# Kernel tuning notes

Measured on AMD Instinct MI355X. Metric: run time of the kernel, lower is better.

## Reference

```python
import jax, jax.numpy as jnp
import numpy as np
import math

B, L, D, H, FF = 4, 1024, 1024, 16, 4096
DH = D // H
EPS = 1e-12


def layer_norm(x, gamma, beta):
    mean = x.mean(-1, keepdims=True)
    var = ((x - mean) ** 2).mean(-1, keepdims=True)  # biased var, matches unbiased=False
    return gamma * (x - mean) / jnp.sqrt(var + EPS) + beta


def setup_inputs() -> dict:
    key = jax.random.key(0)
    ks = jax.random.split(key, 16)
    s = 0.02
    return {
        "x": jax.random.normal(ks[0], (B, L, D), jnp.float32),
        "attn_bias": jax.random.uniform(ks[1], (B, L, L), jnp.float32),
        "src_mask": jax.random.randint(ks[2], (B, L), 0, 2, jnp.int32),
        "wq": jax.random.normal(ks[3], (D, D), jnp.float32) * s,
        "bq": jnp.zeros((D,), jnp.float32),
        "wk": jax.random.normal(ks[4], (D, D), jnp.float32) * s,
        "bk": jnp.zeros((D,), jnp.float32),
        "wv": jax.random.normal(ks[5], (D, D), jnp.float32) * s,
        "bv": jnp.zeros((D,), jnp.float32),
        "wo": jax.random.normal(ks[6], (D, D), jnp.float32) * s,
        "bo": jnp.zeros((D,), jnp.float32),
        "gamma1": jnp.ones((D,), jnp.float32),
        "beta1": jnp.zeros((D,), jnp.float32),
        "w1": jax.random.normal(ks[7], (D, FF), jnp.float32) * s,
        "b1": jnp.zeros((FF,), jnp.float32),
        "w2": jax.random.normal(ks[8], (FF, D), jnp.float32) * s,
        "b2": jnp.zeros((D,), jnp.float32),
        "gamma2": jnp.ones((D,), jnp.float32),
        "beta2": jnp.zeros((D,), jnp.float32),
    }


def reference(x, attn_bias, src_mask, wq, bq, wk, bk, wv, bv, wo, bo,
              gamma1, beta1, w1, b1, w2, b2, gamma2, beta2):
    # ---- multi-head attention with multiplicative bias + additive mask ----
    def split_heads(t):  # [B,L,D] -> [B,H,L,DH]
        return t.reshape(B, L, H, DH).transpose(0, 2, 1, 3)

    q = split_heads(x @ wq + bq)
    k = split_heads(x @ wk + bk)
    v = split_heads(x @ wv + bv)

    score = jnp.einsum('bhqd,bhkd->bhqk', q, k) / math.sqrt(DH)
    score = score * attn_bias[:, None, :, :]               # multiplicative bias
    score = jnp.where(src_mask[:, None, None, :] == 0, -10000.0, score)
    p = jax.nn.softmax(score, axis=-1)
    ctx = jnp.einsum('bhqk,bhkd->bhqd', p, v)
    ctx = ctx.transpose(0, 2, 1, 3).reshape(B, L, D)
    attn_out = ctx @ wo + bo

    h = layer_norm(x + attn_out, gamma1, beta1)

    # ---- position-wise FFN ----
    ffn = jax.nn.relu(h @ w1 + b1) @ w2 + b2
    out = layer_norm(h + ffn, gamma2, beta2)
    return out
```

## Files before the change

### kernel.cpp

```cpp
#include <hip/hip_runtime.h>
#include <hip/hip_bf16.h>
#include <math.h>

#define BB 4
#define LL 1024
#define DD 1024
#define HH 16
#define DHH 64
#define FFF 4096
#define MM (BB*LL)
#define LDQ 3072

typedef __attribute__((ext_vector_type(8))) short short8;
typedef __attribute__((ext_vector_type(4))) float f32x4;

__device__ __forceinline__ ushort f2bf(float f) {
    __hip_bfloat16 h = __float2bfloat16(f);
    return *(ushort*)&h;
}
__device__ __forceinline__ float bf2f(ushort u) {
    __hip_bfloat16 h = *(__hip_bfloat16*)&u;
    return __bfloat162float(h);
}
__device__ __forceinline__ float fexp2(float x) {
#if __has_builtin(__builtin_amdgcn_exp2f)
    return __builtin_amdgcn_exp2f(x);
#else
    return exp2f(x);
#endif
}

__device__ __forceinline__ float block_reduce_sum(float v, float* red, int tid) {
    red[tid] = v;
    __syncthreads();
    for (int off = 128; off > 0; off >>= 1) {
        if (tid < off) red[tid] += red[tid + off];
        __syncthreads();
    }
    float r = red[0];
    __syncthreads();
    return r;
}

__global__ __launch_bounds__(256)
void cast_bf16(const float* __restrict__ in, ushort* __restrict__ out) {
    const int i = blockIdx.x * 256 + threadIdx.x;
    float4 v = ((const float4*)in)[i];
    ushort4 o;
    o.x = f2bf(v.x); o.y = f2bf(v.y); o.z = f2bf(v.z); o.w = f2bf(v.w);
    ((ushort4*)out)[i] = o;
}

__global__ __launch_bounds__(256)
void swizzle_bias(const float* __restrict__ bias, float* __restrict__ B) {
    __shared__ float rowbuf[1024];
    const int row = blockIdx.x;
    const int t = threadIdx.x;
    *(float4*)&rowbuf[t * 4] = *(const float4*)&bias[(size_t)row * 1024 + t * 4];
    __syncthreads();
    const int kt = t >> 4, c = t & 15;
    const float s = 1.4426950408889634f;
    float4 o;
    o.x = rowbuf[kt * 64 + 0 * 16 + c] * s;
    o.y = rowbuf[kt * 64 + 1 * 16 + c] * s;
    o.z = rowbuf[kt * 64 + 2 * 16 + c] * s;
    o.w = rowbuf[kt * 64 + 3 * 16 + c] * s;
    *(float4*)&B[(size_t)row * 1024 + t * 4] = o;
}

__global__ __launch_bounds__(256)
void transpose_cast(const float* __restrict__ W, ushort* __restrict__ WT,
                    int K, int N) {
    __shared__ float tile[32][33];
    const int n0 = blockIdx.x * 32, k0 = blockIdx.y * 32;
    const int t = threadIdx.x;
    const int r = t >> 3, c4 = (t & 7) * 4;
    float4 v = *(const float4*)&W[(size_t)(k0 + r) * N + n0 + c4];
    tile[r][c4 + 0] = v.x; tile[r][c4 + 1] = v.y;
    tile[r][c4 + 2] = v.z; tile[r][c4 + 3] = v.w;
    __syncthreads();
    ushort4 o;
    o.x = f2bf(tile[c4 + 0][r]);
    o.y = f2bf(tile[c4 + 1][r]);
    o.z = f2bf(tile[c4 + 2][r]);
    o.w = f2bf(tile[c4 + 3][r]);
    *(ushort4*)&WT[(size_t)(n0 + r) * K + k0 + c4] = o;
}

__global__ __launch_bounds__(256)
void concat3(const float* __restrict__ a, const float* __restrict__ b,
             const float* __restrict__ c, float* __restrict__ o) {
    const int i = blockIdx.x * 256 + threadIdx.x;
    o[i] = (i < 1024) ? a[i] : ((i < 2048) ? b[i - 1024] : c[i - 2048]);
}

template<int BN>
__global__ __launch_bounds__(256)
void gemm_bf16_sk(const ushort* __restrict__ A, const ushort* __restrict__ Bt,
                  float* __restrict__ P, int M, int N, int K) {
    constexpr int JF = BN / 32;
    __shared__ ushort Als0[128 * 32];
    __shared__ ushort Als1[128 * 32];
    __shared__ ushort Bls0[BN * 32];
    __shared__ ushort Bls1[BN * 32];

    const int L = blockIdx.x + gridDim.x * blockIdx.y;
    const int xcd = L & 7;
    const int idx = L >> 3;
    const int mpx = gridDim.y >> 3;
    const int bm = (xcd * mpx + (idx % mpx)) * 128;
    const int bn = (idx / mpx) * BN;
    const int kbeg = blockIdx.z * (K >> 1);
    const int kend = kbeg + (K >> 1);

    const int t = threadIdx.x;
    const int lane = t & 63;
    const int w = t >> 6;
    const int wm = (w >> 1) * 64;
    const int wn = (w & 1) * (BN / 2);
    const int fm = lane & 15;
    const int kg = lane >> 4;

    f32x4 acc[4][JF] = {};

    for (int k0 = kbeg; k0 < kend; k0 += 64) {
        #pragma unroll
        for (int j = 0; j < 2; ++j) {
            const int chunk = j * 256 + t;
            const int row = chunk >> 2, kc = chunk & 3;
            const ushort* ga0 = A + (size_t)(bm + row) * K + k0 + kc * 8;
            __builtin_amdgcn_global_load_lds(
                (const __attribute__((address_space(1))) void*)ga0,
                (__attribute__((address_space(3))) void*)(Als0 + chunk * 8), 16, 0, 0);
            const ushort* ga1 = ga0 + 32;
            __builtin_amdgcn_global_load_lds(
                (const __attribute__((address_space(1))) void*)ga1,
                (__attribute__((address_space(3))) void*)(Als1 + chunk * 8), 16, 0, 0);
        }
        #pragma unroll
        for (int j = 0; j < BN / 64; ++j) {
            const int chunk = j * 256 + t;
            const int row = chunk >> 2, kc = chunk & 3;
            const ushort* gb0 = Bt + (size_t)(bn + row) * K + k0 + kc * 8;
            __builtin_amdgcn_global_load_lds(
                (const __attribute__((address_space(1))) void*)gb0,
                (__attribute__((address_space(3))) void*)(Bls0 + chunk * 8), 16, 0, 0);
            const ushort* gb1 = gb0 + 32;
            __builtin_amdgcn_global_load_lds(
                (const __attribute__((address_space(1))) void*)gb1,
                (__attribute__((address_space(3))) void*)(Bls1 + chunk * 8), 16, 0, 0);
        }
        __syncthreads();

        short8 af[4][2], bfr[JF][2];
        #pragma unroll
        for (int i = 0; i < 4; ++i) {
            af[i][0] = *(const short8*)&Als0[(wm + i * 16 + fm) * 32 + kg * 8];
            af[i][1] = *(const short8*)&Als1[(wm + i * 16 + fm) * 32 + kg * 8];
        }
        #pragma unroll
        for (int j = 0; j < JF; ++j) {
            bfr[j][0] = *(const short8*)&Bls0[(wn + j * 16 + fm) * 32 + kg * 8];
            bfr[j][1] = *(const short8*)&Bls1[(wn + j * 16 + fm) * 32 + kg * 8];
        }
        #pragma unroll
        for (int i = 0; i < 4; ++i)
            #pragma unroll
            for (int j = 0; j < JF; ++j) {
                acc[i][j] = __builtin_amdgcn_mfma_f32_16x16x32_bf16(
                    af[i][0], bfr[j][0], acc[i][j], 0, 0, 0);
                acc[i][j] = __builtin_amdgcn_mfma_f32_16x16x32_bf16(
                    af[i][1], bfr[j][1], acc[i][j], 0, 0, 0);
            }
        __syncthreads();
    }

    float* Pz = P + (size_t)blockIdx.z * M * N;
    const int orow0 = (lane >> 4) * 4;
    const int ocol = lane & 15;
    #pragma unroll
    for (int j = 0; j < JF; ++j) {
        const int n = bn + wn + j * 16 + ocol;
        #pragma unroll
        for (int i = 0; i < 4; ++i) {
            const int m0 = bm + wm + i * 16 + orow0;
            #pragma unroll
            for (int r = 0; r < 4; ++r)
                Pz[(size_t)(m0 + r) * N + n] = acc[i][j][r];
        }
    }
}


#define BARM() asm volatile("s_barrier" ::: "memory")
#define VMC4() asm volatile("s_waitcnt vmcnt(4)" ::: "memory")
#define LGK0() do { asm volatile("s_waitcnt lgkmcnt(0)" ::: "memory"); \
                    __builtin_amdgcn_sched_barrier(0); } while (0)

__device__ __forceinline__ short8 fragrd(const ushort* h, int row, int s, int kg) {
    const int cb = ((s << 6) + (kg << 4)) ^ ((row & 7) << 4);
    return *(const short8*)(h + row * 64 + (cb >> 1));
}

__device__ __forceinline__ void stage_half(const ushort* __restrict__ src,
                                           int srcK, ushort* ldsh, int t) {
    #pragma unroll
    for (int l = 0; l < 2; ++l) {
        const int chunk = l * 512 + t;
        const int r = chunk >> 3;
        const int cb_log = ((chunk & 7) * 16) ^ ((r & 7) << 4);
        const ushort* g = src + (size_t)r * srcK + (cb_log >> 1);
        __builtin_amdgcn_global_load_lds(
            (const __attribute__((address_space(1))) void*)g,
            (__attribute__((address_space(3))) void*)(ldsh + chunk * 8), 16, 0, 0);
    }
}

__global__ __launch_bounds__(512, 2)
void gemm256(const ushort* __restrict__ A, const ushort* __restrict__ Bt,
             const float* __restrict__ bias, ushort* __restrict__ C,
             ushort* __restrict__ Vt, int vn0,
             int M, int N, int K, int relu, int qlim) {
    __shared__ ushort lds[65536];

    const int nt = K >> 6;
    const int t = threadIdx.x;
    const int lane = t & 63;
    const int w = t >> 6;
    const int wr = w >> 2, wc = w & 3;
    const int fm = lane & 15, kg = lane >> 4;

    const int bid = blockIdx.x;
    const int wg = (bid & 7) * (gridDim.x >> 3) + (bid >> 3);
    const int bm = (wg & 15) << 8;
    const int bn = (wg >> 4) << 8;

    ushort* const A0 = lds;
    ushort* const B0 = lds + 16384;
    ushort* const A1 = lds + 32768;
    ushort* const B1 = lds + 49152;

    const ushort* const Ah0 = A0 + wr * 8192;
    const ushort* const Ah1 = A1 + wr * 8192;
    const ushort* const Bh0 = B0 + (wc >> 1) * 8192;
    const ushort* const Bh1 = B1 + (wc >> 1) * 8192;
    const int brow = (wc & 1) * 64;

    #define ASRC(tt, h) (A  + (size_t)(bm + (h) * 128) * K + (tt) * 64)
    #define BSRC(tt, h) (Bt + (size_t)(bn + (h) * 128) * K + (tt) * 64)

    f32x4 acc[8][4] = {};
    short8 af[4][2];
    short8 bf2[4][2];

    #define RD_A(HP, MI0) do { \
        _Pragma("unroll") \
        for (int i = 0; i < 4; ++i) { \
            const int row = ((MI0) + i) * 16 + fm; \
            af[i][0] = fragrd((HP), row, 0, kg); \
            af[i][1] = fragrd((HP), row, 1, kg); \
        } } while (0)

    #define RD_B(HP, J0) do { \
        _Pragma("unroll") \
        for (int jj = 0; jj < 2; ++jj) { \
            const int row = brow + ((J0) + jj) * 16 + fm; \
            bf2[(J0) + jj][0] = fragrd((HP), row, 0, kg); \
            bf2[(J0) + jj][1] = fragrd((HP), row, 1, kg); \
        } } while (0)

    #define QMFMA(MI0, J0) do { \
        __builtin_amdgcn_s_setprio(1); \
        _Pragma("unroll") \
        for (int i = 0; i < 4; ++i) { \
            _Pragma("unroll") \
            for (int jj = 0; jj < 2; ++jj) { \
                acc[(MI0)+i][(J0)+jj] = __builtin_amdgcn_mfma_f32_16x16x32_bf16( \
                    af[i][0], bf2[(J0)+jj][0], acc[(MI0)+i][(J0)+jj], 0, 0, 0); \
                acc[(MI0)+i][(J0)+jj] = __builtin_amdgcn_mfma_f32_16x16x32_bf16( \
                    af[i][1], bf2[(J0)+jj][1], acc[(MI0)+i][(J0)+jj], 0, 0, 0); \
            } } \
        __builtin_amdgcn_s_setprio(0); \
    } while (0)

    stage_half(BSRC(0, 0), K, B0, t);
    stage_half(BSRC(0, 1), K, B0 + 8192, t);
    stage_half(ASRC(0, 0), K, A0, t);
    stage_half(ASRC(0, 1), K, A0 + 8192, t);
    stage_half(BSRC(1, 0), K, B1, t);
    stage_half(BSRC(1, 1), K, B1 + 8192, t);
    VMC4();
    BARM();

    for (int it = 0; it < (nt >> 1); ++it) {
        const int ta = 2 * it;
        const int tb = ta + 1;
        const int t2 = min(ta + 2, nt - 1);
        const int t3 = min(ta + 3, nt - 1);

        RD_A(Ah0, 0); RD_B(Bh0, 0);
        stage_half(ASRC(tb, 0), K, A1, t);
        BARM(); LGK0(); QMFMA(0, 0); BARM();
        RD_B(Bh0, 2);
        stage_half(ASRC(tb, 1), K, A1 + 8192, t);
        BARM(); LGK0(); QMFMA(0, 2); BARM();
        RD_A(Ah0, 4);
        stage_half(BSRC(t2, 0), K, B0, t);
        BARM(); LGK0(); QMFMA(4, 2); BARM();
        stage_half(BSRC(t2, 1), K, B0 + 8192, t);
        VMC4();
        BARM(); LGK0(); QMFMA(4, 0); BARM();
        RD_A(Ah1, 0); RD_B(Bh1, 0);
        stage_half(ASRC(t2, 0), K, A0, t);
        BARM(); LGK0(); QMFMA(0, 0); BARM();
        RD_B(Bh1, 2);
        stage_half(ASRC(t2, 1), K, A0 + 8192, t);
        BARM(); LGK0(); QMFMA(0, 2); BARM();
        RD_A(Ah1, 4);
        stage_half(BSRC(t3, 0), K, B1, t);
        BARM(); LGK0(); QMFMA(4, 2); BARM();
        stage_half(BSRC(t3, 1), K, B1 + 8192, t);
        VMC4();
        BARM(); LGK0(); QMFMA(4, 0); BARM();
    }

    const int oc = lane & 15, og = lane >> 4;
    #pragma unroll
    for (int nj = 0; nj < 4; ++nj) {
        const int nb = bn + wc * 64 + nj * 16;
        const int n = nb + oc;
        const float bv = bias[n];
        const bool isV = nb >= vn0;
        #pragma unroll
        for (int mi = 0; mi < 8; ++mi) {
            const int m0 = bm + wr * 128 + mi * 16 + og * 4;
            if (isV) {
                ushort4 o;
                o.x = f2bf(acc[mi][nj][0] + bv);
                o.y = f2bf(acc[mi][nj][1] + bv);
                o.z = f2bf(acc[mi][nj][2] + bv);
                o.w = f2bf(acc[mi][nj][3] + bv);
                *(ushort4*)&Vt[((size_t)((m0 >> 10) << 10) + (n - vn0)) * 1024 + (m0 & 1023)] = o;
            } else {
                #pragma unroll
                for (int r = 0; r < 4; ++r) {
                    float v = acc[mi][nj][r] + bv;
                    if (relu) v = fmaxf(v, 0.0f);
                    if (n < qlim) v *= 0.125f;
                    C[(size_t)(m0 + r) * N + n] = f2bf(v);
                }
            }
        }
    }
    #undef ASRC
    #undef BSRC
    #undef RD_A
    #undef RD_B
    #undef QMFMA
}

__global__ __launch_bounds__(256, 4)
void attn_mfma(const ushort* __restrict__ QKVb, const ushort* __restrict__ Vt,
               const float* __restrict__ biasw, const int* __restrict__ mask,
               ushort* __restrict__ ctx) {
    const int q0 = blockIdx.x * 64;
    const int h = blockIdx.y;
    const int b = blockIdx.z;
    const int t = threadIdx.x;
    const int lane = t & 63;
    const int w = t >> 6;
    const int g = lane >> 4;
    const int c = lane & 15;

    __shared__ ushort QP[64 * 72];
    __shared__ ushort Ks[64 * 72];
    __shared__ ushort Vs[64 * 72];
    __shared__ float maskS[LL];

    #pragma unroll
    for (int i = 0; i < 2; ++i) {
        const int chunk = i * 256 + t;
        const int row = chunk >> 3, c8 = (chunk & 7) * 8;
        *(short8*)&QP[row * 72 + c8] =
            *(const short8*)(QKVb + ((size_t)(b * LL + q0 + row)) * LDQ + h * DHH + c8);
    }
    {
        int4 mi = ((const int4*)(mask + b * LL))[t];
        float4 mf;
        mf.x = mi.x ? 0.0f : -49152.0f;
        mf.y = mi.y ? 0.0f : -49152.0f;
        mf.z = mi.z ? 0.0f : -49152.0f;
        mf.w = mi.w ? 0.0f : -49152.0f;
        ((float4*)maskS)[t] = mf;
    }

    short8 pk[2], pv[2];
    #pragma unroll
    for (int i = 0; i < 2; ++i) {
        const int chunk = i * 256 + t;
        const int row = chunk >> 3, c8 = (chunk & 7) * 8;
        pk[i] = *(const short8*)(QKVb + ((size_t)(b * LL + row)) * LDQ + 1024 + h * DHH + c8);
        pv[i] = *(const short8*)(Vt + ((size_t)((b * HH + h) * DHH + row)) * LL + c8);
    }
    __syncthreads();

    short8 aq0 = *(const short8*)&QP[(w * 16 + c) * 72 + g * 8];
    short8 aq1 = *(const short8*)&QP[(w * 16 + c) * 72 + g * 8 + 32];
    ushort* Pw = QP + w * (16 * 72);

    const float* bp = biasw + (size_t)(b * LL + q0 + w * 16 + 4 * g) * 1024 + c * 4;
    float4 pb[4];
    #pragma unroll
    for (int r = 0; r < 4; ++r)
        pb[r] = *(const float4*)(bp + r * 1024);

    float l_run[4] = {0.f, 0.f, 0.f, 0.f};
    f32x4 acc_o[4] = {};

    for (int kt = 0; kt < 16; ++kt) {
        #pragma unroll
        for (int i = 0; i < 2; ++i) {
            const int chunk = i * 256 + t;
            const int row = chunk >> 3, c8 = (chunk & 7) * 8;
            *(short8*)&Ks[row * 72 + c8] = pk[i];
            *(short8*)&Vs[row * 72 + c8] = pv[i];
        }
        __syncthreads();

        if (kt < 15) {
            const int k0n = (kt + 1) * 64;
            #pragma unroll
            for (int i = 0; i < 2; ++i) {
                const int chunk = i * 256 + t;
                const int row = chunk >> 3, c8 = (chunk & 7) * 8;
                pk[i] = *(const short8*)(QKVb + ((size_t)(b * LL + k0n + row)) * LDQ + 1024 + h * DHH + c8);
                pv[i] = *(const short8*)(Vt + ((size_t)((b * HH + h) * DHH + row)) * LL + k0n + c8);
            }
        }

        float4 pbn[4];
        if (kt < 15) {
            #pragma unroll
            for (int r = 0; r < 4; ++r)
                pbn[r] = *(const float4*)(bp + r * 1024 + (kt + 1) * 64);
        }

        float mk[4];
        #pragma unroll
        for (int j = 0; j < 4; ++j) mk[j] = maskS[kt * 64 + j * 16 + c];

        f32x4 accs[4] = {};
        __builtin_amdgcn_s_setprio(1);
        #pragma unroll
        for (int j = 0; j < 4; ++j) {
            short8 bk0 = *(const short8*)&Ks[(j * 16 + c) * 72 + g * 8];
            short8 bk1 = *(const short8*)&Ks[(j * 16 + c) * 72 + g * 8 + 32];
            accs[j] = __builtin_amdgcn_mfma_f32_16x16x32_bf16(aq0, bk0, accs[j], 0, 0, 0);
            accs[j] = __builtin_amdgcn_mfma_f32_16x16x32_bf16(aq1, bk1, accs[j], 0, 0, 0);
        }
        __builtin_amdgcn_s_setprio(0);

        #pragma unroll
        for (int j = 0; j < 4; ++j)
            #pragma unroll
            for (int r = 0; r < 4; ++r) {
                const float pe = fexp2(fmaf(accs[j][r], ((const float*)&pb[r])[j], mk[j]));
                l_run[r] += pe;
                Pw[(4 * g + r) * 72 + j * 16 + c] = f2bf(pe);
            }

        __builtin_amdgcn_s_setprio(1);
        #pragma unroll
        for (int ks = 0; ks < 2; ++ks) {
            short8 ap = *(const short8*)&Pw[c * 72 + ks * 32 + g * 8];
            #pragma unroll
            for (int j = 0; j < 4; ++j) {
                short8 bv8 = *(const short8*)&Vs[(j * 16 + c) * 72 + ks * 32 + g * 8];
                acc_o[j] = __builtin_amdgcn_mfma_f32_16x16x32_bf16(ap, bv8, acc_o[j], 0, 0, 0);
            }
        }
        __builtin_amdgcn_s_setprio(0);

        if (kt < 15) {
            #pragma unroll
            for (int r = 0; r < 4; ++r) pb[r] = pbn[r];
        }
        __syncthreads();
    }

    #pragma unroll
    for (int r = 0; r < 4; ++r) {
        float l = l_run[r];
        #pragma unroll
        for (int d = 1; d < 16; d <<= 1) l += __shfl_xor(l, d);
        const float inv = 1.0f / l;
        #pragma unroll
        for (int j = 0; j < 4; ++j)
            ctx[((size_t)(b * LL + q0 + w * 16 + 4 * g + r)) * DD + h * DHH + j * 16 + c] =
                f2bf(acc_o[j][r] * inv);
    }
}

__global__ __launch_bounds__(256)
void add_ln_kernel(const float* __restrict__ P0, const float* __restrict__ P1,
                   const float* __restrict__ cb, const float* __restrict__ bres,
                   const float* __restrict__ gamma, const float* __restrict__ beta,
                   float* __restrict__ out, ushort* __restrict__ outb) {
    const int row = blockIdx.x;
    const int tid = threadIdx.x;
    __shared__ float red[256];

    const size_t base = (size_t)row * DD;
    float v[4];
    float sum = 0.0f;
    #pragma unroll
    for (int i = 0; i < 4; ++i) {
        const int col = tid + i * 256;
        v[i] = P0[base + col] + P1[base + col] + cb[col] + bres[base + col];
        sum += v[i];
    }
    const float mean = block_reduce_sum(sum, red, tid) * (1.0f / 1024.0f);
    float vs = 0.0f;
    #pragma unroll
    for (int i = 0; i < 4; ++i) {
        const float dlt = v[i] - mean;
        vs += dlt * dlt;
    }
    const float var = block_reduce_sum(vs, red, tid) * (1.0f / 1024.0f);
    const float rstd = rsqrtf(var + 1e-12f);
    #pragma unroll
    for (int i = 0; i < 4; ++i) {
        const int col = tid + i * 256;
        const float o = gamma[col] * (v[i] - mean) * rstd + beta[col];
        out[base + col] = o;
        if (outb) outb[base + col] = f2bf(o);
    }
}

extern "C" void kernel_launch(void* const* d_in, const int* in_sizes, int n_in,
                              void* d_out, int out_size, void* d_ws, size_t ws_size,
                              hipStream_t stream) {
    const float* x         = (const float*)d_in[0];
    const float* attn_bias = (const float*)d_in[1];
    const int*   src_mask  = (const int*)  d_in[2];
    const float* wq = (const float*)d_in[3];
    const float* bq = (const float*)d_in[4];
    const float* wk = (const float*)d_in[5];
    const float* bk = (const float*)d_in[6];
    const float* wv = (const float*)d_in[7];
    const float* bv = (const float*)d_in[8];
    const float* wo = (const float*)d_in[9];
    const float* bo = (const float*)d_in[10];
    const float* gamma1 = (const float*)d_in[11];
    const float* beta1  = (const float*)d_in[12];
    const float* w1 = (const float*)d_in[13];
    const float* b1 = (const float*)d_in[14];
    const float* w2 = (const float*)d_in[15];
    const float* b2 = (const float*)d_in[16];
    const float* gamma2 = (const float*)d_in[17];
    const float* beta2  = (const float*)d_in[18];
    float* out = (float*)d_out;

    const size_t MB = 1024 * 1024;
    char* W = (char*)d_ws;
    ushort* xb    = (ushort*)(W + 0);
    ushort* ctxb  = (ushort*)(W + 0);
    ushort* W1T   = (ushort*)(W + 0);
    ushort* QKVb  = (ushort*)(W + 8 * MB);
    float*  Hb    = (float*) (W + 8 * MB);
    ushort* Hbb   = (ushort*)(W + 24 * MB);
    ushort* W2T   = (ushort*)(W + 24 * MB);
    ushort* F1b   = (ushort*)(W + 32 * MB);
    ushort* Vt    = (ushort*)(W + 40 * MB);
    ushort* WQKVT = (ushort*)(W + 48 * MB);
    ushort* WOT   = (ushort*)(W + 48 * MB);
    float*  bqkv  = (float*) (W + 62 * MB);
    float*  biasw = (float*) (W + 64 * MB);
    float*  P0    = (float*) (W + 64 * MB);

    dim3 blk(256);

    cast_bf16<<<dim3(4096), blk, 0, stream>>>(x, xb);
    swizzle_bias<<<dim3(4096), blk, 0, stream>>>(attn_bias, biasw);
    transpose_cast<<<dim3(32, 32), blk, 0, stream>>>(wq, WQKVT, DD, DD);
    transpose_cast<<<dim3(32, 32), blk, 0, stream>>>(wk, WQKVT + 1024 * 1024, DD, DD);
    transpose_cast<<<dim3(32, 32), blk, 0, stream>>>(wv, WQKVT + 2048 * 1024, DD, DD);
    concat3<<<dim3(12), blk, 0, stream>>>(bq, bk, bv, bqkv);
    gemm256<<<dim3(192), dim3(512), 0, stream>>>(xb, WQKVT, bqkv, QKVb,
                                                 Vt, 2048, MM, LDQ, DD, 0, 1024);
    attn_mfma<<<dim3(16, HH, BB), blk, 0, stream>>>(QKVb, Vt, biasw, src_mask, ctxb);
    transpose_cast<<<dim3(32, 32), blk, 0, stream>>>(wo, WOT, DD, DD);
    gemm_bf16_sk<64><<<dim3(16, 32, 2), blk, 0, stream>>>(ctxb, WOT, P0, MM, DD, DD);
    transpose_cast<<<dim3(128, 32), blk, 0, stream>>>(w1, W1T, DD, FFF);
    add_ln_kernel<<<dim3(MM), blk, 0, stream>>>(P0, P0 + (size_t)MM * DD, bo, x,
                                                gamma1, beta1, Hb, Hbb);
    gemm256<<<dim3(256), dim3(512), 0, stream>>>(Hbb, W1T, b1, F1b,
                                                 Vt, 1 << 30, MM, FFF, DD, 1, 0);
    transpose_cast<<<dim3(32, 128), blk, 0, stream>>>(w2, W2T, FFF, DD);
    gemm_bf16_sk<64><<<dim3(16, 32, 2), blk, 0, stream>>>(F1b, W2T, P0, MM, DD, FFF);
    add_ln_kernel<<<dim3(MM), blk, 0, stream>>>(P0, P0 + (size_t)MM * DD, b2, Hb,
                                                gamma2, beta2, out, nullptr);
}
```

Baseline: 386.7 us.

## Replace split-K and QKV GEMMs with triple-buffered 256x128 swizzled-LDS GEMM

Adds a templated 512-thread GEMM with a 256x128 output tile, a three-stage LDS ring fed by async global-to-LDS loads, XOR-swizzled fragment reads and priority-raised MFMA phases. It replaces the simple double-buffer-free split-K kernel used for the output projection and second FFN GEMM, and also replaces gemm256 for the fused QKV projection, using 384 tiles instead of 192 for better CU coverage. The goal is to hide load latency and cut LDS bank conflicts; in exchange it uses a large LDS footprint (~144KB) which limits occupancy.

```diff
diff --git a/kernel.cpp b/kernel.cpp
--- a/kernel.cpp
+++ b/kernel.cpp
@@ -94,106 +94,10 @@
     o[i] = (i < 1024) ? a[i] : ((i < 2048) ? b[i - 1024] : c[i - 2048]);
 }
 
-template<int BN>
-__global__ __launch_bounds__(256)
-void gemm_bf16_sk(const ushort* __restrict__ A, const ushort* __restrict__ Bt,
-                  float* __restrict__ P, int M, int N, int K) {
-    constexpr int JF = BN / 32;
-    __shared__ ushort Als0[128 * 32];
-    __shared__ ushort Als1[128 * 32];
-    __shared__ ushort Bls0[BN * 32];
-    __shared__ ushort Bls1[BN * 32];
-
-    const int L = blockIdx.x + gridDim.x * blockIdx.y;
-    const int xcd = L & 7;
-    const int idx = L >> 3;
-    const int mpx = gridDim.y >> 3;
-    const int bm = (xcd * mpx + (idx % mpx)) * 128;
-    const int bn = (idx / mpx) * BN;
-    const int kbeg = blockIdx.z * (K >> 1);
-    const int kend = kbeg + (K >> 1);
-
-    const int t = threadIdx.x;
-    const int lane = t & 63;
-    const int w = t >> 6;
-    const int wm = (w >> 1) * 64;
-    const int wn = (w & 1) * (BN / 2);
-    const int fm = lane & 15;
-    const int kg = lane >> 4;
-
-    f32x4 acc[4][JF] = {};
-
-    for (int k0 = kbeg; k0 < kend; k0 += 64) {
-        #pragma unroll
-        for (int j = 0; j < 2; ++j) {
-            const int chunk = j * 256 + t;
-            const int row = chunk >> 2, kc = chunk & 3;
-            const ushort* ga0 = A + (size_t)(bm + row) * K + k0 + kc * 8;
-            __builtin_amdgcn_global_load_lds(
-                (const __attribute__((address_space(1))) void*)ga0,
-                (__attribute__((address_space(3))) void*)(Als0 + chunk * 8), 16, 0, 0);
-            const ushort* ga1 = ga0 + 32;
-            __builtin_amdgcn_global_load_lds(
-                (const __attribute__((address_space(1))) void*)ga1,
-                (__attribute__((address_space(3))) void*)(Als1 + chunk * 8), 16, 0, 0);
-        }
-        #pragma unroll
-        for (int j = 0; j < BN / 64; ++j) {
-            const int chunk = j * 256 + t;
-            const int row = chunk >> 2, kc = chunk & 3;
-            const ushort* gb0 = Bt + (size_t)(bn + row) * K + k0 + kc * 8;
-            __builtin_amdgcn_global_load_lds(
-                (const __attribute__((address_space(1))) void*)gb0,
-                (__attribute__((address_space(3))) void*)(Bls0 + chunk * 8), 16, 0, 0);
-            const ushort* gb1 = gb0 + 32;
-            __builtin_amdgcn_global_load_lds(
-                (const __attribute__((address_space(1))) void*)gb1,
-                (__attribute__((address_space(3))) void*)(Bls1 + chunk * 8), 16, 0, 0);
-        }
-        __syncthreads();
-
-        short8 af[4][2], bfr[JF][2];
-        #pragma unroll
-        for (int i = 0; i < 4; ++i) {
-            af[i][0] = *(const short8*)&Als0[(wm + i * 16 + fm) * 32 + kg * 8];
-            af[i][1] = *(const short8*)&Als1[(wm + i * 16 + fm) * 32 + kg * 8];
-        }
-        #pragma unroll
-        for (int j = 0; j < JF; ++j) {
-            bfr[j][0] = *(const short8*)&Bls0[(wn + j * 16 + fm) * 32 + kg * 8];
-            bfr[j][1] = *(const short8*)&Bls1[(wn + j * 16 + fm) * 32 + kg * 8];
-        }
-        #pragma unroll
-        for (int i = 0; i < 4; ++i)
-            #pragma unroll
-            for (int j = 0; j < JF; ++j) {
-                acc[i][j] = __builtin_amdgcn_mfma_f32_16x16x32_bf16(
-                    af[i][0], bfr[j][0], acc[i][j], 0, 0, 0);
-                acc[i][j] = __builtin_amdgcn_mfma_f32_16x16x32_bf16(
-                    af[i][1], bfr[j][1], acc[i][j], 0, 0, 0);
-            }
-        __syncthreads();
-    }
-
-    float* Pz = P + (size_t)blockIdx.z * M * N;
-    const int orow0 = (lane >> 4) * 4;
-    const int ocol = lane & 15;
-    #pragma unroll
-    for (int j = 0; j < JF; ++j) {
-        const int n = bn + wn + j * 16 + ocol;
-        #pragma unroll
-        for (int i = 0; i < 4; ++i) {
-            const int m0 = bm + wm + i * 16 + orow0;
-            #pragma unroll
-            for (int r = 0; r < 4; ++r)
-                Pz[(size_t)(m0 + r) * N + n] = acc[i][j][r];
-        }
-    }
-}
-
 
 #define BARM() asm volatile("s_barrier" ::: "memory")
 #define VMC4() asm volatile("s_waitcnt vmcnt(4)" ::: "memory")
+#define VMC6() asm volatile("s_waitcnt vmcnt(6)" ::: "memory")
 #define LGK0() do { asm volatile("s_waitcnt lgkmcnt(0)" ::: "memory"); \
                     __builtin_amdgcn_sched_barrier(0); } while (0)
 
@@ -359,6 +263,147 @@
     #undef QMFMA
 }
 
+template<int MODE>
+__global__ __launch_bounds__(512, 2)
+void gemm_hk128(const ushort* __restrict__ A, const ushort* __restrict__ Bt,
+                const float* __restrict__ bias, void* __restrict__ C,
+                ushort* __restrict__ Vt, int vn0,
+                int M, int N, int K, int qlim) {
+    __shared__ ushort lds[73728];
+    ushort* const SA = lds;
+    ushort* const SB = lds + 49152;
+
+    const int z = blockIdx.y;
+    const int kspan = K / gridDim.y;
+    const int kbeg = z * kspan;
+    const int nt = kspan >> 6;
+
+    const int t = threadIdx.x;
+    const int lane = t & 63;
+    const int w = t >> 6;
+    const int wr = w >> 1, wc = w & 1;
+    const int fm = lane & 15, kg = lane >> 4;
+
+    const int bid = blockIdx.x;
+    const int wg = (bid & 7) * (gridDim.x >> 3) + (bid >> 3);
+    const int bm = (wg & 15) << 8;
+    const int bn = (wg >> 4) << 7;
+
+    const int ahalf = wr >> 1;
+    const int arow0 = (wr & 1) * 64;
+    const int brow0 = wc * 64;
+
+    #define HASRC(tt, h) (A  + (size_t)(bm + (h) * 128) * K + kbeg + (tt) * 64)
+    #define HBSRC(tt)    (Bt + (size_t)bn * K + kbeg + (tt) * 64)
+
+    f32x4 acc[4][4] = {};
+    short8 af[4][2], bf[4][2];
+
+    #define H_RDA(BUFI) do { \
+        const ushort* hp = SA + (BUFI) * 16384 + ahalf * 8192; \
+        _Pragma("unroll") \
+        for (int mi = 0; mi < 4; ++mi) { \
+            const int row = arow0 + mi * 16 + fm; \
+            af[mi][0] = fragrd(hp, row, 0, kg); \
+            af[mi][1] = fragrd(hp, row, 1, kg); \
+        } } while (0)
+
+    #define H_RDB(BUFI, J0) do { \
+        const ushort* hp = SB + (BUFI) * 8192; \
+        _Pragma("unroll") \
+        for (int jj = 0; jj < 2; ++jj) { \
+            const int row = brow0 + ((J0) + jj) * 16 + fm; \
+            bf[(J0) + jj][0] = fragrd(hp, row, 0, kg); \
+            bf[(J0) + jj][1] = fragrd(hp, row, 1, kg); \
+        } } while (0)
+
+    #define H_MFMA(J0) do { \
+        __builtin_amdgcn_s_setprio(1); \
+        _Pragma("unroll") \
+        for (int mi = 0; mi < 4; ++mi) { \
+            _Pragma("unroll") \
+            for (int jj = 0; jj < 2; ++jj) { \
+                acc[mi][(J0)+jj] = __builtin_amdgcn_mfma_f32_16x16x32_bf16( \
+                    af[mi][0], bf[(J0)+jj][0], acc[mi][(J0)+jj], 0, 0, 0); \
+                acc[mi][(J0)+jj] = __builtin_amdgcn_mfma_f32_16x16x32_bf16( \
+                    af[mi][1], bf[(J0)+jj][1], acc[mi][(J0)+jj], 0, 0, 0); \
+            } } \
+        __builtin_amdgcn_s_setprio(0); \
+    } while (0)
+
+    stage_half(HASRC(0, 0), K, SA, t);
+    stage_half(HASRC(0, 1), K, SA + 8192, t);
+    stage_half(HBSRC(0), K, SB, t);
+    stage_half(HASRC(1, 0), K, SA + 16384, t);
+    stage_half(HASRC(1, 1), K, SA + 16384 + 8192, t);
+    stage_half(HBSRC(1), K, SB + 8192, t);
+    VMC6();
+    BARM();
+
+    for (int tt = 0; tt < nt; ++tt) {
+        const int cb = tt % 3;
+        const int tp2 = min(tt + 2, nt - 1);
+        const int sb = tp2 % 3;
+        H_RDA(cb); H_RDB(cb, 0);
+        stage_half(HASRC(tp2, 0), K, SA + sb * 16384, t);
+        stage_half(HASRC(tp2, 1), K, SA + sb * 16384 + 8192, t);
+        stage_half(HBSRC(tp2), K, SB + sb * 8192, t);
+        BARM(); LGK0(); H_MFMA(0); BARM();
+        H_RDB(cb, 2);
+        VMC6();
+        BARM(); LGK0(); H_MFMA(2); BARM();
+    }
+
+    const int oc = lane & 15, og = lane >> 4;
+    if (MODE == 0) {
+        float* Pz = (float*)C + (size_t)z * M * N;
+        #pragma unroll
+        for (int nj = 0; nj < 4; ++nj) {
+            const int n = bn + wc * 64 + nj * 16 + oc;
+            #pragma unroll
+            for (int mi = 0; mi < 4; ++mi) {
+                const int m0 = bm + wr * 64 + mi * 16 + og * 4;
+                #pragma unroll
+                for (int r = 0; r < 4; ++r)
+                    Pz[(size_t)(m0 + r) * N + n] = acc[mi][nj][r];
+            }
+        }
+    } else {
+        ushort* Cb = (ushort*)C;
+        #pragma unroll
+        for (int nj = 0; nj < 4; ++nj) {
+            const int nb = bn + wc * 64 + nj * 16;
+            const int n = nb + oc;
+            const float bv = bias[n];
+            const bool isV = nb >= vn0;
+            #pragma unroll
+            for (int mi = 0; mi < 4; ++mi) {
+                const int m0 = bm + wr * 64 + mi * 16 + og * 4;
+                if (isV) {
+                    ushort4 o;
+                    o.x = f2bf(acc[mi][nj][0] + bv);
+                    o.y = f2bf(acc[mi][nj][1] + bv);
+                    o.z = f2bf(acc[mi][nj][2] + bv);
+                    o.w = f2bf(acc[mi][nj][3] + bv);
+                    *(ushort4*)&Vt[((size_t)((m0 >> 10) << 10) + (n - vn0)) * 1024 + (m0 & 1023)] = o;
+                } else {
+                    #pragma unroll
+                    for (int r = 0; r < 4; ++r) {
+                        float v = acc[mi][nj][r] + bv;
+                        if (n < qlim) v *= 0.125f;
+                        Cb[(size_t)(m0 + r) * N + n] = f2bf(v);
+                    }
+                }
+            }
+        }
+    }
+    #undef HASRC
+    #undef HBSRC
+    #undef H_RDA
+    #undef H_RDB
+    #undef H_MFMA
+}
+
 __global__ __launch_bounds__(256, 4)
 void attn_mfma(const ushort* __restrict__ QKVb, const ushort* __restrict__ Vt,
                const float* __restrict__ biasw, const int* __restrict__ mask,
@@ -586,18 +631,20 @@
     transpose_cast<<<dim3(32, 32), blk, 0, stream>>>(wk, WQKVT + 1024 * 1024, DD, DD);
     transpose_cast<<<dim3(32, 32), blk, 0, stream>>>(wv, WQKVT + 2048 * 1024, DD, DD);
     concat3<<<dim3(12), blk, 0, stream>>>(bq, bk, bv, bqkv);
-    gemm256<<<dim3(192), dim3(512), 0, stream>>>(xb, WQKVT, bqkv, QKVb,
-                                                 Vt, 2048, MM, LDQ, DD, 0, 1024);
+    gemm_hk128<1><<<dim3(384, 1), dim3(512), 0, stream>>>(
+        xb, WQKVT, bqkv, QKVb, Vt, 2048, MM, LDQ, DD, 1024);
     attn_mfma<<<dim3(16, HH, BB), blk, 0, stream>>>(QKVb, Vt, biasw, src_mask, ctxb);
     transpose_cast<<<dim3(32, 32), blk, 0, stream>>>(wo, WOT, DD, DD);
-    gemm_bf16_sk<64><<<dim3(16, 32, 2), blk, 0, stream>>>(ctxb, WOT, P0, MM, DD, DD);
+    gemm_hk128<0><<<dim3(128, 2), dim3(512), 0, stream>>>(
+        ctxb, WOT, nullptr, P0, nullptr, 0, MM, DD, DD, 0);
     transpose_cast<<<dim3(128, 32), blk, 0, stream>>>(w1, W1T, DD, FFF);
     add_ln_kernel<<<dim3(MM), blk, 0, stream>>>(P0, P0 + (size_t)MM * DD, bo, x,
                                                 gamma1, beta1, Hb, Hbb);
     gemm256<<<dim3(256), dim3(512), 0, stream>>>(Hbb, W1T, b1, F1b,
                                                  Vt, 1 << 30, MM, FFF, DD, 1, 0);
     transpose_cast<<<dim3(32, 128), blk, 0, stream>>>(w2, W2T, FFF, DD);
-    gemm_bf16_sk<64><<<dim3(16, 32, 2), blk, 0, stream>>>(F1b, W2T, P0, MM, DD, FFF);
+    gemm_hk128<0><<<dim3(128, 2), dim3(512), 0, stream>>>(
+        F1b, W2T, nullptr, P0, nullptr, 0, MM, DD, FFF, 0);
     add_ln_kernel<<<dim3(MM), blk, 0, stream>>>(P0, P0 + (size_t)MM * DD, b2, Hb,
                                                 gamma2, beta2, out, nullptr);
 }
```

Result: no change. 389.2 us (+0.6%).
